# Kernel tuning notes

Hardware: AMD Instinct MI355X
Metric: run time of the kernel (lower is better)

The kernel has to match this reference:

```python
import jax, jax.numpy as jnp
import numpy as np
import math

K = 7
PAD = 3

def _aniso_kernel(k, sigma_h, sigma_v, angle):
    ax = np.linspace(-(k // 2), k // 2, k, dtype=np.float32)
    xx, yy = np.meshgrid(ax, ax, indexing='ij')
    x_rot = xx * math.cos(angle) + yy * math.sin(angle)
    y_rot = -xx * math.sin(angle) + yy * math.cos(angle)
    ker = np.exp(-(x_rot ** 2 / (2 * sigma_h ** 2) + y_rot ** 2 / (2 * sigma_v ** 2)))
    ker = ker / (ker.sum() + 1e-8)
    return jnp.asarray(ker, dtype=jnp.float32)  # (k,k)

BASE_H = _aniso_kernel(K, 2.5, 1.0, 0.0)
BASE_V = _aniso_kernel(K, 2.5, 1.0, math.pi / 2)

def setup_inputs() -> dict:
    key = jax.random.key(0)
    k1, k2, k3, k4 = jax.random.split(key, 4)
    B, C, H, W, MID = 8, 256, 128, 128, 16
    x = jax.random.normal(k1, (B, C, H, W), dtype=jnp.float32)
    angle_map = jax.random.uniform(k2, (B, H, W), dtype=jnp.float32) * math.pi
    w_reduce = jax.random.normal(k3, (MID, C), dtype=jnp.float32) * 0.05
    w_expand = jax.random.normal(k4, (C, MID), dtype=jnp.float32) * 0.05
    return {"x": x, "angle_map": angle_map, "w_reduce": w_reduce, "w_expand": w_expand}

def reference(x, angle_map, w_reduce, w_expand):
    B, C, H, W = x.shape
    # 1x1 conv reduce: (B,C,H,W) x (mid,C) -> (B,mid,H,W)
    x_low = jnp.einsum('bchw,mc->bmhw', x, w_reduce)
    # per-pixel blend weights
    w_h = jnp.cos(angle_map) ** 2                      # (B,H,W)
    combined = (w_h[..., None, None] * BASE_H
                + (1.0 - w_h)[..., None, None] * BASE_V)  # (B,H,W,k,k)
    combined = combined.reshape(B, H, W, K * K)
    # reflect pad and extract kxk patches (stride 1 -> output spatial == H,W)
    x_pad = jnp.pad(x_low, ((0, 0), (0, 0), (PAD, PAD), (PAD, PAD)), mode='reflect')
    patches = jnp.stack(
        [x_pad[:, :, i:i + H, j:j + W] for i in range(K) for j in range(K)],
        axis=-1)                                       # (B,mid,H,W,k*k)
    out_low = jnp.einsum('bmhwk,bhwk->bmhw', patches, combined)
    out_low = jnp.nan_to_num(out_low)
    out = jnp.einsum('bmhw,cm->bchw', out_low, w_expand)
    return jnp.nan_to_num(out)
```

## Files before the change

kernel.cpp:

```cpp
#include <hip/hip_runtime.h>

#define Bn   8
#define Cn   256
#define MIDn 16
#define Hn   128
#define Wn   128
#define HWn  (Hn * Wn)

__global__ __launch_bounds__(256) void reduce_part_k(const float2* __restrict__ x2,
                                                     const float* __restrict__ wr,
                                                     float2* __restrict__ part2,
                                                     int cper) {
    const int tid = threadIdx.x;
    const int p   = blockIdx.x * 256 + tid;
    const int t   = blockIdx.y;
    const int b   = blockIdx.z;
    const int c0  = t * cper;

    const float2* xb = x2 + ((size_t)b * Cn + c0) * (HWn / 2) + p;

    float2 acc[MIDn];
#pragma unroll
    for (int m = 0; m < MIDn; ++m) acc[m] = make_float2(0.f, 0.f);

#pragma unroll 8
    for (int c = 0; c < cper; ++c) {
        const float2 v = xb[(size_t)c * (HWn / 2)];
        const float* w = wr + (c0 + c);
#pragma unroll
        for (int m = 0; m < MIDn; ++m) {
            const float wm = w[m * Cn];
            acc[m].x = fmaf(v.x, wm, acc[m].x);
            acc[m].y = fmaf(v.y, wm, acc[m].y);
        }
    }

    float2* ob = part2 + ((size_t)t * Bn + b) * MIDn * (HWn / 2) + p;
#pragma unroll
    for (int m = 0; m < MIDn; ++m) ob[(size_t)m * (HWn / 2)] = acc[m];
}

#define TW 32
#define TH 8
#define HR (TH + 6)
#define WR (TW + 6)
#define MH 4

__device__ __forceinline__ int reflect_i(int i, int n) {
    return i < 0 ? -i : (i >= n ? 2 * n - 2 - i : i);
}

__global__ __launch_bounds__(256) void conv_k(const float* __restrict__ part,
                                              const float* __restrict__ ang,
                                              float* __restrict__ xlow2,
                                              int nch) {
    __shared__ float tile[MH][HR][WR];

    const int tid = threadIdx.x;
    const int b   = blockIdx.z;
    const int m0  = blockIdx.y * MH;
    const int rem = blockIdx.x;
    const int th0 = (rem >> 2) * TH;
    const int tw0 = (rem & 3) * TW;

    const size_t chunkF = (size_t)Bn * MIDn * HWn;
    const float* pb = part + (size_t)b * MIDn * HWn + (size_t)m0 * HWn;

    for (int idx = tid; idx < MH * HR * WR; idx += 256) {
        const int m  = idx / (HR * WR);
        const int r2 = idx - m * (HR * WR);
        const int r  = r2 / WR;
        const int cc = r2 - r * WR;
        const int gr = reflect_i(th0 + r - 3, Hn);
        const int gc = reflect_i(tw0 + cc - 3, Wn);
        const size_t off = (size_t)m * HWn + gr * Wn + gc;
        float s = pb[off];
        for (int t = 1; t < nch; ++t) s += pb[(size_t)t * chunkF + off];
        tile[m][r][cc] = s;
    }
    __syncthreads();

    const int pc = tid & (TW - 1);
    const int pr = tid >> 5;
    const int gh = th0 + pr;
    const int gw = tw0 + pc;

    const float a  = ang[b * HWn + gh * Wn + gw];
    const float ch = cosf(a);
    const float wh = ch * ch;

    const float fu[7] = {0.48675226f, 0.72614904f, 0.92311635f, 1.0f,
                         0.92311635f, 0.72614904f, 0.48675226f};
    const float fv[7] = {0.011108997f, 0.13533528f, 0.60653066f, 1.0f,
                         0.60653066f, 0.13533528f, 0.011108997f};
    const float su = 1.f + 2.f * (0.48675226f + 0.72614904f + 0.92311635f);
    const float sv = 1.f + 2.f * (0.011108997f + 0.13533528f + 0.60653066f);
    const float inv = 1.f / (su * sv + 1e-8f);
    const float aH = wh * inv;
    const float aV = (1.f - wh) * inv;

    float wcomb[49];
#pragma unroll
    for (int i = 0; i < 7; ++i)
#pragma unroll
        for (int j = 0; j < 7; ++j)
            wcomb[i * 7 + j] = aH * (fu[i] * fv[j]) + aV * (fv[i] * fu[j]);

    float* ob = xlow2 + (size_t)b * MIDn * HWn + (size_t)m0 * HWn + gh * Wn + gw;
#pragma unroll
    for (int m = 0; m < MH; ++m) {
        float acc = 0.f;
#pragma unroll
        for (int i = 0; i < 7; ++i)
#pragma unroll
            for (int j = 0; j < 7; ++j)
                acc = fmaf(wcomb[i * 7 + j], tile[m][pr + i][pc + j], acc);
        ob[(size_t)m * HWn] = acc;
    }
}

__global__ __launch_bounds__(256) void expand_k(const float2* __restrict__ xlow22,
                                                const float* __restrict__ we,
                                                float2* __restrict__ out2) {
    const int tid = threadIdx.x;
    const int p   = blockIdx.x * 256 + tid;
    const int c0  = blockIdx.y * 64;
    const int b   = blockIdx.z;

    const float2* xb = xlow22 + (size_t)b * MIDn * (HWn / 2) + p;
    float2 ol[MIDn];
#pragma unroll
    for (int m = 0; m < MIDn; ++m) ol[m] = xb[(size_t)m * (HWn / 2)];

    float2* ob = out2 + ((size_t)b * Cn + c0) * (HWn / 2) + p;
#pragma unroll 4
    for (int ci = 0; ci < 64; ++ci) {
        const float* w = we + (size_t)(c0 + ci) * MIDn;
        float2 o = make_float2(0.f, 0.f);
#pragma unroll
        for (int m = 0; m < MIDn; ++m) {
            o.x = fmaf(w[m], ol[m].x, o.x);
            o.y = fmaf(w[m], ol[m].y, o.y);
        }
        ob[(size_t)ci * (HWn / 2)] = o;
    }
}

extern "C" void kernel_launch(void* const* d_in, const int* in_sizes, int n_in,
                              void* d_out, int out_size, void* d_ws, size_t ws_size,
                              hipStream_t stream) {
    const float* x   = (const float*)d_in[0];
    const float* ang = (const float*)d_in[1];
    const float* wr  = (const float*)d_in[2];
    const float* we  = (const float*)d_in[3];
    float*       out = (float*)d_out;

    const size_t chunkB = (size_t)Bn * MIDn * HWn * sizeof(float);
    const int nch = (ws_size >= 5 * chunkB) ? 4 : 1;
    float* part  = (float*)d_ws;
    float* xlow2 = (float*)((char*)d_ws + (size_t)nch * chunkB);

    reduce_part_k<<<dim3(32, nch, Bn), dim3(256), 0, stream>>>(
        (const float2*)x, wr, (float2*)part, Cn / nch);
    conv_k<<<dim3(64, MIDn / MH, Bn), dim3(256), 0, stream>>>(part, ang, xlow2, nch);
    expand_k<<<dim3(32, Cn / 64, Bn), dim3(256), 0, stream>>>(
        (const float2*)xlow2, we, (float2*)out);
}
```

Measured before the change: 284.6 us.

## Fuse conv with expand and reduce channel partials in shared memory

The reduce kernel now splits the 256 input channels across the four waves of one block and sums their partial results in LDS. This removes the global partial buffers and the multi-chunk re-read in the conv stage. The conv kernel now handles all 16 mid channels per tile and directly computes the 256-channel expand output. That drops the separate expand kernel and the round-trip of the intermediate through memory. In exchange the fused kernel uses a much larger LDS tile and has only 512 blocks, each writing 256 channels serially, so occupancy and parallelism drop.

After: 314.7 us. 1.11x slower.

```diff
diff --git a/kernel.cpp b/kernel.cpp
--- a/kernel.cpp
+++ b/kernel.cpp
@@ -7,24 +7,27 @@
 #define Wn   128
 #define HWn  (Hn * Wn)
 
-__global__ __launch_bounds__(256) void reduce_part_k(const float2* __restrict__ x2,
-                                                     const float* __restrict__ wr,
-                                                     float2* __restrict__ part2,
-                                                     int cper) {
+__global__ __launch_bounds__(256, 4) void reduce_k(const float2* __restrict__ x2,
+                                                   const float* __restrict__ wr,
+                                                   float2* __restrict__ xlow2) {
+    __shared__ float2 comb[4][MIDn][64];
+
     const int tid = threadIdx.x;
-    const int p   = blockIdx.x * 256 + tid;
-    const int t   = blockIdx.y;
-    const int b   = blockIdx.z;
-    const int c0  = t * cper;
+    const int p2  = tid & 63;
+    const int wv  = tid >> 6;
+    const int b   = blockIdx.y;
+    const int p0  = blockIdx.x * 64;
 
-    const float2* xb = x2 + ((size_t)b * Cn + c0) * (HWn / 2) + p;
+    const int c0 = __builtin_amdgcn_readfirstlane(wv << 6);
+
+    const float2* xb = x2 + ((size_t)b * Cn + c0) * (HWn / 2) + p0 + p2;
 
     float2 acc[MIDn];
 #pragma unroll
     for (int m = 0; m < MIDn; ++m) acc[m] = make_float2(0.f, 0.f);
 
 #pragma unroll 8
-    for (int c = 0; c < cper; ++c) {
+    for (int c = 0; c < 64; ++c) {
         const float2 v = xb[(size_t)c * (HWn / 2)];
         const float* w = wr + (c0 + c);
 #pragma unroll
@@ -35,48 +38,57 @@
         }
     }
 
-    float2* ob = part2 + ((size_t)t * Bn + b) * MIDn * (HWn / 2) + p;
 #pragma unroll
-    for (int m = 0; m < MIDn; ++m) ob[(size_t)m * (HWn / 2)] = acc[m];
+    for (int m = 0; m < MIDn; ++m) comb[wv][m][p2] = acc[m];
+    __syncthreads();
+
+    float2* ob = xlow2 + (size_t)b * MIDn * (HWn / 2) + p0;
+#pragma unroll
+    for (int k = 0; k < 4; ++k) {
+        const int idx = k * 256 + tid;
+        const int m   = idx >> 6;
+        const int q   = idx & 63;
+        const float2 s0 = comb[0][m][q];
+        const float2 s1 = comb[1][m][q];
+        const float2 s2 = comb[2][m][q];
+        const float2 s3 = comb[3][m][q];
+        float2 s;
+        s.x = (s0.x + s1.x) + (s2.x + s3.x);
+        s.y = (s0.y + s1.y) + (s2.y + s3.y);
+        ob[(size_t)m * (HWn / 2) + q] = s;
+    }
 }
 
 #define TW 32
 #define TH 8
 #define HR (TH + 6)
 #define WR (TW + 6)
-#define MH 4
 
 __device__ __forceinline__ int reflect_i(int i, int n) {
     return i < 0 ? -i : (i >= n ? 2 * n - 2 - i : i);
 }
 
-__global__ __launch_bounds__(256) void conv_k(const float* __restrict__ part,
-                                              const float* __restrict__ ang,
-                                              float* __restrict__ xlow2,
-                                              int nch) {
-    __shared__ float tile[MH][HR][WR];
+__global__ __launch_bounds__(256, 2) void conv_expand_k(const float* __restrict__ xlow,
+                                                        const float* __restrict__ ang,
+                                                        const float* __restrict__ we,
+                                                        float* __restrict__ out) {
+    __shared__ float tile[MIDn][HR][WR];
 
     const int tid = threadIdx.x;
-    const int b   = blockIdx.z;
-    const int m0  = blockIdx.y * MH;
+    const int b   = blockIdx.y;
     const int rem = blockIdx.x;
     const int th0 = (rem >> 2) * TH;
     const int tw0 = (rem & 3) * TW;
 
-    const size_t chunkF = (size_t)Bn * MIDn * HWn;
-    const float* pb = part + (size_t)b * MIDn * HWn + (size_t)m0 * HWn;
-
-    for (int idx = tid; idx < MH * HR * WR; idx += 256) {
+    const float* pb = xlow + (size_t)b * MIDn * HWn;
+    for (int idx = tid; idx < MIDn * HR * WR; idx += 256) {
         const int m  = idx / (HR * WR);
         const int r2 = idx - m * (HR * WR);
         const int r  = r2 / WR;
         const int cc = r2 - r * WR;
         const int gr = reflect_i(th0 + r - 3, Hn);
         const int gc = reflect_i(tw0 + cc - 3, Wn);
-        const size_t off = (size_t)m * HWn + gr * Wn + gc;
-        float s = pb[off];
-        for (int t = 1; t < nch; ++t) s += pb[(size_t)t * chunkF + off];
-        tile[m][r][cc] = s;
+        tile[m][r][cc] = pb[(size_t)m * HWn + gr * Wn + gc];
     }
     __syncthreads();
 
@@ -85,7 +97,7 @@
     const int gh = th0 + pr;
     const int gw = tw0 + pc;
 
-    const float a  = ang[b * HWn + gh * Wn + gw];
+    const float a  = ang[(size_t)b * HWn + gh * Wn + gw];
     const float ch = cosf(a);
     const float wh = ch * ch;
 
@@ -106,43 +118,26 @@
         for (int j = 0; j < 7; ++j)
             wcomb[i * 7 + j] = aH * (fu[i] * fv[j]) + aV * (fv[i] * fu[j]);
 
-    float* ob = xlow2 + (size_t)b * MIDn * HWn + (size_t)m0 * HWn + gh * Wn + gw;
+    float low[MIDn];
 #pragma unroll
-    for (int m = 0; m < MH; ++m) {
+    for (int m = 0; m < MIDn; ++m) {
         float acc = 0.f;
 #pragma unroll
         for (int i = 0; i < 7; ++i)
 #pragma unroll
             for (int j = 0; j < 7; ++j)
                 acc = fmaf(wcomb[i * 7 + j], tile[m][pr + i][pc + j], acc);
-        ob[(size_t)m * HWn] = acc;
+        low[m] = acc;
     }
-}
 
-__global__ __launch_bounds__(256) void expand_k(const float2* __restrict__ xlow22,
-                                                const float* __restrict__ we,
-                                                float2* __restrict__ out2) {
-    const int tid = threadIdx.x;
-    const int p   = blockIdx.x * 256 + tid;
-    const int c0  = blockIdx.y * 64;
-    const int b   = blockIdx.z;
-
-    const float2* xb = xlow22 + (size_t)b * MIDn * (HWn / 2) + p;
-    float2 ol[MIDn];
+    float* ob = out + (size_t)b * Cn * HWn + gh * Wn + gw;
+#pragma unroll 4
+    for (int c = 0; c < Cn; ++c) {
+        const float* w = we + (size_t)c * MIDn;
+        float o = 0.f;
 #pragma unroll
-    for (int m = 0; m < MIDn; ++m) ol[m] = xb[(size_t)m * (HWn / 2)];
-
-    float2* ob = out2 + ((size_t)b * Cn + c0) * (HWn / 2) + p;
-#pragma unroll 4
-    for (int ci = 0; ci < 64; ++ci) {
-        const float* w = we + (size_t)(c0 + ci) * MIDn;
-        float2 o = make_float2(0.f, 0.f);
-#pragma unroll
-        for (int m = 0; m < MIDn; ++m) {
-            o.x = fmaf(w[m], ol[m].x, o.x);
-            o.y = fmaf(w[m], ol[m].y, o.y);
-        }
-        ob[(size_t)ci * (HWn / 2)] = o;
+        for (int m = 0; m < MIDn; ++m) o = fmaf(w[m], low[m], o);
+        ob[(size_t)c * HWn] = o;
     }
 }
 
@@ -155,14 +150,9 @@
     const float* we  = (const float*)d_in[3];
     float*       out = (float*)d_out;
 
-    const size_t chunkB = (size_t)Bn * MIDn * HWn * sizeof(float);
-    const int nch = (ws_size >= 5 * chunkB) ? 4 : 1;
-    float* part  = (float*)d_ws;
-    float* xlow2 = (float*)((char*)d_ws + (size_t)nch * chunkB);
+    float* xlow = (float*)d_ws;
 
-    reduce_part_k<<<dim3(32, nch, Bn), dim3(256), 0, stream>>>(
-        (const float2*)x, wr, (float2*)part, Cn / nch);
-    conv_k<<<dim3(64, MIDn / MH, Bn), dim3(256), 0, stream>>>(part, ang, xlow2, nch);
-    expand_k<<<dim3(32, Cn / 64, Bn), dim3(256), 0, stream>>>(
-        (const float2*)xlow2, we, (float2*)out);
+    reduce_k<<<dim3((HWn / 2) / 64, Bn), dim3(256), 0, stream>>>(
+        (const float2*)x, wr, (float2*)xlow);
+    conv_expand_k<<<dim3(64, Bn), dim3(256), 0, stream>>>(xlow, ang, we, out);
 }
```
